# Kernel optimization log

Hardware: AMD Instinct MI355X
Metric: run time of the kernel (lower is better)

The kernel has to match this reference:

```python
import jax, jax.numpy as jnp
import numpy as np

B, S, HID = 2, 2048, 1024
H, D = 16, 64  # head_dim = HID // H
MAXPOS = 2048


def setup_inputs() -> dict:
    key = jax.random.key(0)
    ks = jax.random.split(key, 9)
    s = 0.02
    return {
        "hidden_states": jax.random.normal(ks[0], (B, S, HID), jnp.float32),
        "attention_mask": jnp.zeros((B, 1, 1, S), jnp.float32),
        "Wq": jax.random.normal(ks[1], (HID, HID), jnp.float32) * s,
        "bq": jnp.zeros((HID,), jnp.float32),
        "Wk": jax.random.normal(ks[2], (HID, HID), jnp.float32) * s,
        "bk": jnp.zeros((HID,), jnp.float32),
        "Wv": jax.random.normal(ks[3], (HID, HID), jnp.float32) * s,
        "bv": jnp.zeros((HID,), jnp.float32),
        "dist_emb": jax.random.normal(ks[4], (2 * MAXPOS - 1, D), jnp.float32) * s,
    }


def reference(hidden_states, attention_mask, Wq, bq, Wk, bk, Wv, bv, dist_emb):
    b, s, _ = hidden_states.shape

    def heads(x):  # [B,S,HID] -> [B,H,S,D]
        return x.reshape(b, s, H, D).transpose(0, 2, 1, 3)

    q = heads(hidden_states @ Wq.T + bq)
    k = heads(hidden_states @ Wk.T + bk)
    v = heads(hidden_states @ Wv.T + bv)

    # raw scores [B,H,L,R]
    scores = jnp.einsum("bhld,bhrd->bhlr", q, k)

    # relative_key_query position bias
    pos_l = jnp.arange(s)[:, None]
    pos_r = jnp.arange(s)[None, :]
    distance = pos_l - pos_r + (MAXPOS - 1)  # [L,R]
    pos_emb = dist_emb[distance]  # [L,R,D]
    rel_q = jnp.einsum("bhld,lrd->bhlr", q, pos_emb)
    rel_k = jnp.einsum("bhrd,lrd->bhlr", k, pos_emb)
    scores = scores + rel_q + rel_k

    scores = scores / jnp.sqrt(jnp.asarray(D, scores.dtype))
    scores = scores + attention_mask  # additive mask broadcast [B,1,1,R]

    probs = jax.nn.softmax(scores, axis=-1)  # dropout p=0 -> identity
    ctx = jnp.einsum("bhlr,bhrd->bhld", probs, v)  # [B,H,L,D]
    ctx = ctx.transpose(0, 2, 1, 3).reshape(b, s, H * D)
    return ctx
```

## Files before the change

kernel.cpp:

```cpp
#include <hip/hip_runtime.h>

typedef __bf16 bf16_t;
typedef __bf16 bf16x8 __attribute__((ext_vector_type(8)));
typedef __bf16 bf16x4v __attribute__((ext_vector_type(4)));
typedef float floatx4 __attribute__((ext_vector_type(4)));

#define MFMA16(a, b, c) __builtin_amdgcn_mfma_f32_16x16x32_bf16((a), (b), (c), 0, 0, 0)

constexpr int S_ = 2048;
constexpr int HID_ = 1024;
constexpr int HH = 16;
constexpr int DD = 64;
constexpr float ALPHA = 0.125f * 1.44269504f;
constexpr float LOG2E = 1.44269504f;

__device__ __forceinline__ void async_copy16(const bf16_t* g, bf16_t* l) {
  __builtin_amdgcn_global_load_lds((const __attribute__((address_space(1))) unsigned int*)g,
                                   (__attribute__((address_space(3))) unsigned int*)l, 16, 0, 0);
}

__global__ __launch_bounds__(256) void cvt_all_kernel(
    const float* __restrict__ h, const float* __restrict__ wq, const float* __restrict__ wk,
    const float* __restrict__ wv, const float* __restrict__ de, bf16_t* __restrict__ hb,
    bf16_t* __restrict__ wb, bf16_t* __restrict__ eb) {
  int v = blockIdx.x * 256 + threadIdx.x;
  if (v >= 1900528) return;
  const float* src;
  bf16_t* dst;
  int off;
  if (v < 1048576) {
    src = h; dst = hb; off = v;
  } else if (v < 1310720) {
    src = wq; dst = wb; off = v - 1048576;
  } else if (v < 1572864) {
    src = wk; dst = wb + 1048576; off = v - 1310720;
  } else if (v < 1835008) {
    src = wv; dst = wb + 2097152; off = v - 1572864;
  } else {
    src = de; dst = eb; off = v - 1835008;
  }
  float4 f = *(const float4*)(src + (size_t)off * 4);
  bf16x4v p = {(bf16_t)f.x, (bf16_t)f.y, (bf16_t)f.z, (bf16_t)f.w};
  *(bf16x4v*)(dst + (size_t)off * 4) = p;
}

__global__ __launch_bounds__(256) void cvt_e_kernel(const float* __restrict__ src,
                                                    bf16_t* __restrict__ dst, int n) {
  int i = blockIdx.x * 256 + threadIdx.x;
  if (i < n) dst[i] = (bf16_t)src[i];
}

__global__ __launch_bounds__(256) void qkv_gemm4_kernel(
    const bf16_t* __restrict__ hb, const bf16_t* __restrict__ wb,
    const float* __restrict__ bq, const float* __restrict__ bk, const float* __restrict__ bv,
    bf16_t* __restrict__ qb, bf16_t* __restrict__ kb, bf16_t* __restrict__ vb) {
  __shared__ alignas(16) bf16_t As[128 * 64];
  __shared__ alignas(16) bf16_t Bs[128 * 64];
  const int tid = threadIdx.x;
  const int lane = tid & 63, wid = tid >> 6;
  const int l15 = lane & 15, quad = lane >> 4;
  const int bidx = blockIdx.x;
  const int xcd = bidx & 7, idx = bidx >> 3;
  const int m0 = (xcd * 4 + (idx & 3)) * 128;
  const int nAbs = (idx >> 2) * 128;
  const int wm = (wid >> 1) * 64, wn = (wid & 1) * 64;
  floatx4 acc[4][4] = {};
  const int srow = wid * 8 + (lane >> 3);
  const int scol = (lane & 7) * 8;
  const bf16_t* aptr = hb + (size_t)(m0 + srow) * HID_ + scol;
  const bf16_t* bptr = wb + (size_t)(nAbs + srow) * HID_ + scol;
  bf16_t* As_w = As + (size_t)(wid * 8) * 64;
  bf16_t* Bs_w = Bs + (size_t)(wid * 8) * 64;

  for (int k0 = 0; k0 < HID_; k0 += 64) {
    __syncthreads();
#pragma unroll
    for (int p = 0; p < 4; ++p) {
      async_copy16(aptr + k0 + (size_t)p * 32 * HID_, As_w + p * 32 * 64);
      async_copy16(bptr + k0 + (size_t)p * 32 * HID_, Bs_w + p * 32 * 64);
    }
    __syncthreads();
    bf16x8 af[4][2], bfv[4][2];
#pragma unroll
    for (int t = 0; t < 4; ++t)
#pragma unroll
      for (int kh = 0; kh < 2; ++kh) {
        af[t][kh] = *(const bf16x8*)&As[(wm + t * 16 + l15) * 64 + kh * 32 + quad * 8];
        bfv[t][kh] = *(const bf16x8*)&Bs[(wn + t * 16 + l15) * 64 + kh * 32 + quad * 8];
      }
#pragma unroll
    for (int mt = 0; mt < 4; ++mt)
#pragma unroll
      for (int nt = 0; nt < 4; ++nt) {
        acc[mt][nt] = MFMA16(af[mt][0], bfv[nt][0], acc[mt][nt]);
        acc[mt][nt] = MFMA16(af[mt][1], bfv[nt][1], acc[mt][nt]);
      }
  }

  const int z = nAbs >> 10;
  const float* bias = (z == 0) ? bq : (z == 1) ? bk : bv;
  bf16_t* out = (z == 0) ? qb : (z == 1) ? kb : vb;
  const float scl = (z == 0) ? ALPHA : 1.0f;
#pragma unroll
  for (int nt = 0; nt < 4; ++nt) {
    int oo = (nAbs & 1023) + wn + nt * 16 + l15;
    float bvs = bias[oo];
    int h = oo >> 6, d = oo & 63;
#pragma unroll
    for (int mt = 0; mt < 4; ++mt) {
      int sb = m0 + wm + mt * 16 + quad * 4;
      int b = sb >> 11, s = sb & 2047;
      if (z != 2) {
        bf16_t* dst = out + (((size_t)(b * HH + h) * S_ + s) * DD + d);
#pragma unroll
        for (int i = 0; i < 4; ++i) dst[(size_t)i * DD] = (bf16_t)((acc[mt][nt][i] + bvs) * scl);
      } else {
        bf16_t* dst = out + (((size_t)(b * HH + h) * DD + d) * S_ + s);
        bf16x4v pk = {(bf16_t)(acc[mt][nt][0] + bvs), (bf16_t)(acc[mt][nt][1] + bvs),
                      (bf16_t)(acc[mt][nt][2] + bvs), (bf16_t)(acc[mt][nt][3] + bvs)};
        *(bf16x4v*)dst = pk;
      }
    }
  }
}

__global__ __launch_bounds__(256) void qkv_gemm_kernel(
    const float* __restrict__ X, const float* __restrict__ W,
    const float* __restrict__ bias, bf16_t* __restrict__ out, int transposed, float scl) {
  __shared__ alignas(16) bf16_t As[128][40];
  __shared__ alignas(16) bf16_t Bs[128][40];
  const int tid = threadIdx.x;
  const int lane = tid & 63, wid = tid >> 6;
  const int l15 = lane & 15, quad = lane >> 4;
  const int m0 = blockIdx.x * 128, n0 = blockIdx.y * 128;
  const int wm = (wid >> 1) * 64, wn = (wid & 1) * 64;
  floatx4 acc[4][4] = {};
  const int srow = tid >> 1, scol = (tid & 1) * 16;
  const float* aptr = X + (size_t)(m0 + srow) * HID_ + scol;
  const float* bptr = W + (size_t)(n0 + srow) * HID_ + scol;

  for (int k0 = 0; k0 < HID_; k0 += 32) {
    __syncthreads();
    {
      const float4* a4 = (const float4*)(aptr + k0);
      float4 f0 = a4[0], f1 = a4[1], f2 = a4[2], f3 = a4[3];
      bf16x4v p0 = {(bf16_t)f0.x, (bf16_t)f0.y, (bf16_t)f0.z, (bf16_t)f0.w};
      bf16x4v p1 = {(bf16_t)f1.x, (bf16_t)f1.y, (bf16_t)f1.z, (bf16_t)f1.w};
      bf16x4v p2 = {(bf16_t)f2.x, (bf16_t)f2.y, (bf16_t)f2.z, (bf16_t)f2.w};
      bf16x4v p3 = {(bf16_t)f3.x, (bf16_t)f3.y, (bf16_t)f3.z, (bf16_t)f3.w};
      *(bf16x4v*)&As[srow][scol + 0] = p0;
      *(bf16x4v*)&As[srow][scol + 4] = p1;
      *(bf16x4v*)&As[srow][scol + 8] = p2;
      *(bf16x4v*)&As[srow][scol + 12] = p3;
      const float4* b4 = (const float4*)(bptr + k0);
      float4 g0 = b4[0], g1 = b4[1], g2 = b4[2], g3 = b4[3];
      bf16x4v q0 = {(bf16_t)g0.x, (bf16_t)g0.y, (bf16_t)g0.z, (bf16_t)g0.w};
      bf16x4v q1 = {(bf16_t)g1.x, (bf16_t)g1.y, (bf16_t)g1.z, (bf16_t)g1.w};
      bf16x4v q2 = {(bf16_t)g2.x, (bf16_t)g2.y, (bf16_t)g2.z, (bf16_t)g2.w};
      bf16x4v q3 = {(bf16_t)g3.x, (bf16_t)g3.y, (bf16_t)g3.z, (bf16_t)g3.w};
      *(bf16x4v*)&Bs[srow][scol + 0] = q0;
      *(bf16x4v*)&Bs[srow][scol + 4] = q1;
      *(bf16x4v*)&Bs[srow][scol + 8] = q2;
      *(bf16x4v*)&Bs[srow][scol + 12] = q3;
    }
    __syncthreads();
    bf16x8 af[4], bfv[4];
#pragma unroll
    for (int t = 0; t < 4; ++t) af[t] = *(const bf16x8*)&As[wm + t * 16 + l15][quad * 8];
#pragma unroll
    for (int t = 0; t < 4; ++t) bfv[t] = *(const bf16x8*)&Bs[wn + t * 16 + l15][quad * 8];
#pragma unroll
    for (int mt = 0; mt < 4; ++mt)
#pragma unroll
      for (int nt = 0; nt < 4; ++nt)
        acc[mt][nt] = MFMA16(af[mt], bfv[nt], acc[mt][nt]);
  }

#pragma unroll
  for (int nt = 0; nt < 4; ++nt) {
    int o = n0 + wn + nt * 16 + l15;
    float bv = bias[o];
    int h = o >> 6, d = o & 63;
#pragma unroll
    for (int mt = 0; mt < 4; ++mt) {
      int sb = m0 + wm + mt * 16 + quad * 4;
      int b = sb >> 11, s = sb & 2047;
      if (!transposed) {
        bf16_t* dst = out + (((size_t)(b * HH + h) * S_ + s) * DD + d);
#pragma unroll
        for (int i = 0; i < 4; ++i) dst[(size_t)i * DD] = (bf16_t)((acc[mt][nt][i] + bv) * scl);
      } else {
        bf16_t* dst = out + (((size_t)(b * HH + h) * DD + d) * S_ + s);
        bf16x4v pk = {(bf16_t)(acc[mt][nt][0] + bv), (bf16_t)(acc[mt][nt][1] + bv),
                      (bf16_t)(acc[mt][nt][2] + bv), (bf16_t)(acc[mt][nt][3] + bv)};
        *(bf16x4v*)dst = pk;
      }
    }
  }
}

__global__ __launch_bounds__(256, 3) void attn8_kernel(
    const bf16_t* __restrict__ Q, const bf16_t* __restrict__ K,
    const bf16_t* __restrict__ Vt, const bf16_t* __restrict__ E,
    const float* __restrict__ mask, float* __restrict__ out) {
  __shared__ alignas(16) bf16_t Er[128 * 64];
  __shared__ alignas(16) bf16_t Vs[64 * 64];
  __shared__ alignas(16) bf16_t PX[65 * 64];
  __shared__ alignas(16) bf16_t X1t[64][134];
  __shared__ float lsumS[4][64];

  const int tid = threadIdx.x;
  const int lane = tid & 63, wid = tid >> 6;
  const int l15 = lane & 15, quad = lane >> 4;
  const int bh = blockIdx.x & 31, lblk = blockIdx.x >> 5;
  const int l0 = lblk * 64;
  const bf16_t* Qb = Q + (size_t)bh * S_ * DD;
  const bf16_t* Kb = K + (size_t)bh * S_ * DD;
  const bf16_t* Vb = Vt + (size_t)bh * DD * S_;
  const float* maskb = mask + (size_t)(bh >> 4) * S_;

  bf16x8 qB[4][2];
#pragma unroll
  for (int ct = 0; ct < 4; ++ct) {
    const bf16_t* qp = Qb + (size_t)(l0 + ct * 16 + l15) * DD + quad * 8;
    qB[ct][0] = *(const bf16x8*)qp;
    qB[ct][1] = *(const bf16x8*)(qp + 32);
  }

  {
    int rr = tid >> 2, c0 = (tid & 3) * 2;
    int grow = l0 + 2048 + rr;
    if (grow > 4094) grow = 4094;
    const bf16_t* ep = E + (size_t)grow * DD + c0 * 8;
    bf16x8 e0 = *(const bf16x8*)ep;
    bf16x8 e1 = *(const bf16x8*)(ep + 8);
    int slot = (l0 + 2048 + rr) & 127, sw = rr & 7;
    *(bf16x8*)&Er[slot * 64 + (((c0 + 0) ^ sw) << 3)] = e0;
    *(bf16x8*)&Er[slot * 64 + (((c0 + 1) ^ sw) << 3)] = e1;
  }
  __syncthreads();

#pragma unroll
  for (int wt = 0; wt < 4; ++wt) {
    int sr = (l0 + 2048 + wt * 16 + l15) & 127;
    int sw = l15 & 7;
    bf16x8 e0 = *(const bf16x8*)&Er[sr * 64 + ((quad ^ sw) << 3)];
    bf16x8 e1 = *(const bf16x8*)&Er[sr * 64 + (((4 + quad) ^ sw) << 3)];
    floatx4 t1 = {};
    t1 = MFMA16(qB[wid][0], e0, t1);
    t1 = MFMA16(qB[wid][1], e1, t1);
    const int wl = wt * 16 + l15;
#pragma unroll
    for (int i = 0; i < 4; ++i) {
      int ll = wid * 16 + quad * 4 + i;
      int r = ll - wl - 1;
      int col = (r >= 0) ? r : (128 + i);
      X1t[ll][col] = (bf16_t)t1[i];
    }
  }

  floatx4 Oacc[4] = {};
  float lsum[4] = {0.f, 0.f, 0.f, 0.f};

  for (int r0 = 0; r0 < S_; r0 += 64) {
    const int A = l0 - r0 + 1984;
    {
      int rr = tid >> 2, c0 = (tid & 3) * 2;
      const bf16_t* ep = E + (size_t)(A + rr) * DD + c0 * 8;
      bf16x8 e0 = *(const bf16x8*)ep;
      bf16x8 e1 = *(const bf16x8*)(ep + 8);
      int slot = (A + rr) & 127, sw = rr & 7;
      *(bf16x8*)&Er[slot * 64 + (((c0 + 0) ^ sw) << 3)] = e0;
      *(bf16x8*)&Er[slot * 64 + (((c0 + 1) ^ sw) << 3)] = e1;
    }
    const bf16_t* kp = Kb + (size_t)(r0 + wid * 16 + l15) * DD + quad * 8;
    bf16x8 kf0 = *(const bf16x8*)kp;
    bf16x8 kf1 = *(const bf16x8*)(kp + 32);
    float4 m4 = *(const float4*)(maskb + r0 + wid * 16 + quad * 4);
    float mlg[4] = {m4.x * LOG2E, m4.y * LOG2E, m4.z * LOG2E, m4.w * LOG2E};
    __syncthreads();

#pragma unroll
    for (int wt = 0; wt < 8; ++wt) {
      const bool needT1 = (wt < 4);
      const bool needT2 = (wt + wid >= 3) && (wt + wid <= 7);
      if (!(needT1 || needT2)) continue;
      int sr = (A + wt * 16 + l15) & 127;
      int sw = l15 & 7;
      bf16x8 e0 = *(const bf16x8*)&Er[sr * 64 + ((quad ^ sw) << 3)];
      bf16x8 e1 = *(const bf16x8*)&Er[sr * 64 + (((4 + quad) ^ sw) << 3)];
      const int wl = wt * 16 + l15;
      if (needT2) {
        floatx4 t2 = {};
        t2 = MFMA16(kf0, e0, t2);
        t2 = MFMA16(kf1, e1, t2);
#pragma unroll
        for (int i = 0; i < 4; ++i) {
          int rl = wid * 16 + quad * 4 + i;
          int ll = rl + wl - 63;
          int row = ((unsigned)ll < 64u) ? ll : 64;
          int col = (((rl >> 3) ^ (row & 7)) << 3) + (rl & 7);
          PX[row * 64 + col] = (bf16_t)(t2[i] * ALPHA + mlg[i]);
        }
      }
      if (needT1) {
        floatx4 t1 = {};
        t1 = MFMA16(qB[wid][0], e0, t1);
        t1 = MFMA16(qB[wid][1], e1, t1);
#pragma unroll
        for (int i = 0; i < 4; ++i) {
          int ll = wid * 16 + quad * 4 + i;
          int rc = (r0 + 63 + ll - wl) & 127;
          X1t[ll][rc] = (bf16_t)t1[i];
        }
      }
    }
    {
      int row = tid >> 2, c0 = (tid & 3) * 2;
      const bf16_t* vp = Vb + (size_t)row * S_ + r0 + c0 * 8;
      bf16x8 v0 = *(const bf16x8*)vp;
      bf16x8 v1 = *(const bf16x8*)(vp + 8);
      int h7 = row & 7;
      *(bf16x8*)&Vs[row * 64 + (((c0 + 0) ^ h7) << 3)] = v0;
      *(bf16x8*)&Vs[row * 64 + (((c0 + 1) ^ h7) << 3)] = v1;
    }
    __syncthreads();

    const int xc = (r0 + wid * 16 + quad * 4) & 127;
    const int pc = wid * 2 + (quad >> 1);
#pragma unroll
    for (int ct = 0; ct < 4; ++ct) {
      floatx4 s = {};
      s = MFMA16(kf0, qB[ct][0], s);
      s = MFMA16(kf1, qB[ct][1], s);
      bf16x4v x1 = *(const bf16x4v*)&X1t[ct * 16 + l15][xc];
      const int row = ct * 16 + l15;
      bf16_t* px = &PX[row * 64 + (((pc ^ (row & 7)) << 3) + ((quad & 1) << 2))];
      bf16x4v x2 = *(const bf16x4v*)px;
      bf16x4v pk;
#pragma unroll
      for (int i = 0; i < 4; ++i) {
        float sv = s[i] + (float)x1[i] + (float)x2[i];
        float p = __builtin_amdgcn_exp2f(sv);
        lsum[ct] += p;
        pk[i] = (bf16_t)p;
      }
      *(bf16x4v*)px = pk;
    }
    __syncthreads();

    {
      const int prow = wid * 16 + l15;
      const int ph = prow & 7;
      bf16x8 pf0 = *(const bf16x8*)&PX[prow * 64 + ((quad ^ ph) << 3)];
      bf16x8 pf1 = *(const bf16x8*)&PX[prow * 64 + (((4 + quad) ^ ph) << 3)];
#pragma unroll
      for (int dt = 0; dt < 4; ++dt) {
        int vrow = dt * 16 + l15;
        int vh = vrow & 7;
        bf16x8 v0 = *(const bf16x8*)&Vs[vrow * 64 + ((quad ^ vh) << 3)];
        bf16x8 v1 = *(const bf16x8*)&Vs[vrow * 64 + (((4 + quad) ^ vh) << 3)];
        Oacc[dt] = MFMA16(v0, pf0, Oacc[dt]);
        Oacc[dt] = MFMA16(v1, pf1, Oacc[dt]);
      }
    }
  }

#pragma unroll
  for (int ct = 0; ct < 4; ++ct) {
    lsum[ct] += __shfl_xor(lsum[ct], 16);
    lsum[ct] += __shfl_xor(lsum[ct], 32);
  }
  __syncthreads();
  if (quad == 0) {
#pragma unroll
    for (int ct = 0; ct < 4; ++ct) lsumS[wid][ct * 16 + l15] = lsum[ct];
  }
  __syncthreads();
  const int lidx = wid * 16 + l15;
  float tot = lsumS[0][lidx] + lsumS[1][lidx] + lsumS[2][lidx] + lsumS[3][lidx];
  float inv = 1.f / tot;
  const int b = bh >> 4, h = bh & 15;
  float* dst = out + (size_t)(b * S_ + l0 + lidx) * HID_ + h * DD + quad * 4;
#pragma unroll
  for (int dt = 0; dt < 4; ++dt) {
    float4 o = {Oacc[dt][0] * inv, Oacc[dt][1] * inv, Oacc[dt][2] * inv, Oacc[dt][3] * inv};
    *(float4*)(dst + dt * 16) = o;
  }
}

extern "C" void kernel_launch(void* const* d_in, const int* in_sizes, int n_in,
                              void* d_out, int out_size, void* d_ws, size_t ws_size,
                              hipStream_t stream) {
  const float* hidden = (const float*)d_in[0];
  const float* amask = (const float*)d_in[1];
  const float* Wq = (const float*)d_in[2];
  const float* bq = (const float*)d_in[3];
  const float* Wk = (const float*)d_in[4];
  const float* bk = (const float*)d_in[5];
  const float* Wv = (const float*)d_in[6];
  const float* bv = (const float*)d_in[7];
  const float* de = (const float*)d_in[8];
  float* outp = (float*)d_out;
  char* ws = (char*)d_ws;
  const size_t MB = 1024 * 1024;
  bf16_t* qb = (bf16_t*)(ws);
  bf16_t* kb = (bf16_t*)(ws + 8 * MB);
  bf16_t* vb = (bf16_t*)(ws + 16 * MB);
  bf16_t* eb = (bf16_t*)(ws + 24 * MB);
  bf16_t* hb = (bf16_t*)(ws + 25 * MB);
  bf16_t* wb = (bf16_t*)(ws + 33 * MB);

  if (ws_size >= 39 * MB) {
    cvt_all_kernel<<<dim3(7424), 256, 0, stream>>>(hidden, Wq, Wk, Wv, de, hb, wb, eb);
    qkv_gemm4_kernel<<<dim3(768), 256, 0, stream>>>(hb, wb, bq, bk, bv, qb, kb, vb);
  } else {
    cvt_e_kernel<<<dim3(1024), 256, 0, stream>>>(de, eb, 4095 * 64);
    dim3 g(32, 8);
    qkv_gemm_kernel<<<g, 256, 0, stream>>>(hidden, Wq, bq, qb, 0, ALPHA);
    qkv_gemm_kernel<<<g, 256, 0, stream>>>(hidden, Wk, bk, kb, 0, 1.0f);
    qkv_gemm_kernel<<<g, 256, 0, stream>>>(hidden, Wv, bv, vb, 1, 1.0f);
  }
  attn8_kernel<<<dim3(1024), 256, 0, stream>>>(qb, kb, vb, eb, amask, outp);
}
```

Measured before the change: 303.5 us.

## Shrink attention LDS footprint by computing query-position bias per tile

The rolling 128-column X1t buffer and the prologue that precomputed the first query-position bias tile are replaced by a 64x64 swizzled X1b buffer that is fully recomputed each key tile. needT1 now selects only the diagonal band of E tiles that each wave needs. The padding row of PX and the separate lsum array are removed, with lsum reusing the Vs buffer. The smaller LDS footprint lets launch bounds ask for 4 blocks per CU instead of 3. The trade-off is that the higher occupancy target may squeeze registers and cause spills.

```diff
diff --git a/kernel.cpp b/kernel.cpp
--- a/kernel.cpp
+++ b/kernel.cpp
@@ -199,15 +199,15 @@
   }
 }
 
-__global__ __launch_bounds__(256, 3) void attn8_kernel(
+__global__ __launch_bounds__(256, 4) void attn11_kernel(
     const bf16_t* __restrict__ Q, const bf16_t* __restrict__ K,
     const bf16_t* __restrict__ Vt, const bf16_t* __restrict__ E,
     const float* __restrict__ mask, float* __restrict__ out) {
   __shared__ alignas(16) bf16_t Er[128 * 64];
   __shared__ alignas(16) bf16_t Vs[64 * 64];
-  __shared__ alignas(16) bf16_t PX[65 * 64];
-  __shared__ alignas(16) bf16_t X1t[64][134];
-  __shared__ float lsumS[4][64];
+  __shared__ alignas(16) bf16_t PX[64 * 64];
+  __shared__ alignas(16) bf16_t X1b[64 * 64];
+  float* lsumS = (float*)Vs;
 
   const int tid = threadIdx.x;
   const int lane = tid & 63, wid = tid >> 6;
@@ -238,26 +238,6 @@
     *(bf16x8*)&Er[slot * 64 + (((c0 + 0) ^ sw) << 3)] = e0;
     *(bf16x8*)&Er[slot * 64 + (((c0 + 1) ^ sw) << 3)] = e1;
   }
-  __syncthreads();
-
-#pragma unroll
-  for (int wt = 0; wt < 4; ++wt) {
-    int sr = (l0 + 2048 + wt * 16 + l15) & 127;
-    int sw = l15 & 7;
-    bf16x8 e0 = *(const bf16x8*)&Er[sr * 64 + ((quad ^ sw) << 3)];
-    bf16x8 e1 = *(const bf16x8*)&Er[sr * 64 + (((4 + quad) ^ sw) << 3)];
-    floatx4 t1 = {};
-    t1 = MFMA16(qB[wid][0], e0, t1);
-    t1 = MFMA16(qB[wid][1], e1, t1);
-    const int wl = wt * 16 + l15;
-#pragma unroll
-    for (int i = 0; i < 4; ++i) {
-      int ll = wid * 16 + quad * 4 + i;
-      int r = ll - wl - 1;
-      int col = (r >= 0) ? r : (128 + i);
-      X1t[ll][col] = (bf16_t)t1[i];
-    }
-  }
 
   floatx4 Oacc[4] = {};
   float lsum[4] = {0.f, 0.f, 0.f, 0.f};
@@ -282,8 +262,8 @@
 
 #pragma unroll
     for (int wt = 0; wt < 8; ++wt) {
-      const bool needT1 = (wt < 4);
       const bool needT2 = (wt + wid >= 3) && (wt + wid <= 7);
+      const bool needT1 = (wt >= wid) && (wt <= wid + 4);
       if (!(needT1 || needT2)) continue;
       int sr = (A + wt * 16 + l15) & 127;
       int sw = l15 & 7;
@@ -298,9 +278,9 @@
         for (int i = 0; i < 4; ++i) {
           int rl = wid * 16 + quad * 4 + i;
           int ll = rl + wl - 63;
-          int row = ((unsigned)ll < 64u) ? ll : 64;
-          int col = (((rl >> 3) ^ (row & 7)) << 3) + (rl & 7);
-          PX[row * 64 + col] = (bf16_t)(t2[i] * ALPHA + mlg[i]);
+          if ((unsigned)ll < 64u)
+            PX[ll * 64 + ((((rl >> 3) ^ (ll & 7)) << 3) + (rl & 7))] =
+                (bf16_t)(t2[i] * ALPHA + mlg[i]);
         }
       }
       if (needT1) {
@@ -310,8 +290,9 @@
 #pragma unroll
         for (int i = 0; i < 4; ++i) {
           int ll = wid * 16 + quad * 4 + i;
-          int rc = (r0 + 63 + ll - wl) & 127;
-          X1t[ll][rc] = (bf16_t)t1[i];
+          int rl = 63 + ll - wl;
+          if ((unsigned)rl < 64u)
+            X1b[ll * 64 + ((((rl >> 3) ^ (ll & 7)) << 3) + (rl & 7))] = (bf16_t)t1[i];
         }
       }
     }
@@ -326,17 +307,16 @@
     }
     __syncthreads();
 
-    const int xc = (r0 + wid * 16 + quad * 4) & 127;
     const int pc = wid * 2 + (quad >> 1);
 #pragma unroll
     for (int ct = 0; ct < 4; ++ct) {
       floatx4 s = {};
       s = MFMA16(kf0, qB[ct][0], s);
       s = MFMA16(kf1, qB[ct][1], s);
-      bf16x4v x1 = *(const bf16x4v*)&X1t[ct * 16 + l15][xc];
       const int row = ct * 16 + l15;
-      bf16_t* px = &PX[row * 64 + (((pc ^ (row & 7)) << 3) + ((quad & 1) << 2))];
-      bf16x4v x2 = *(const bf16x4v*)px;
+      const int off = row * 64 + (((pc ^ (row & 7)) << 3) + ((quad & 1) << 2));
+      bf16x4v x1 = *(const bf16x4v*)&X1b[off];
+      bf16x4v x2 = *(const bf16x4v*)&PX[off];
       bf16x4v pk;
 #pragma unroll
       for (int i = 0; i < 4; ++i) {
@@ -345,7 +325,7 @@
         lsum[ct] += p;
         pk[i] = (bf16_t)p;
       }
-      *(bf16x4v*)px = pk;
+      *(bf16x4v*)&PX[off] = pk;
     }
     __syncthreads();
 
@@ -374,11 +354,11 @@
   __syncthreads();
   if (quad == 0) {
 #pragma unroll
-    for (int ct = 0; ct < 4; ++ct) lsumS[wid][ct * 16 + l15] = lsum[ct];
+    for (int ct = 0; ct < 4; ++ct) lsumS[wid * 64 + ct * 16 + l15] = lsum[ct];
   }
   __syncthreads();
   const int lidx = wid * 16 + l15;
-  float tot = lsumS[0][lidx] + lsumS[1][lidx] + lsumS[2][lidx] + lsumS[3][lidx];
+  float tot = lsumS[lidx] + lsumS[64 + lidx] + lsumS[128 + lidx] + lsumS[192 + lidx];
   float inv = 1.f / tot;
   const int b = bh >> 4, h = bh & 15;
   float* dst = out + (size_t)(b * S_ + l0 + lidx) * HID_ + h * DD + quad * 4;
@@ -421,5 +401,5 @@
     qkv_gemm_kernel<<<g, 256, 0, stream>>>(hidden, Wk, bk, kb, 0, 1.0f);
     qkv_gemm_kernel<<<g, 256, 0, stream>>>(hidden, Wv, bv, vb, 1, 1.0f);
   }
-  attn8_kernel<<<dim3(1024), 256, 0, stream>>>(qb, kb, vb, eb, amask, outp);
-}
+  attn11_kernel<<<dim3(1024), 256, 0, stream>>>(qb, kb, vb, eb, amask, outp);
+}
```

Result: slower. 542.5 us (+78.7%).
